# Kernel optimization log

Measured on AMD Instinct MI355X. Metric: run time of the kernel, lower is better.

Reference implementation:

```python
import jax, jax.numpy as jnp
import numpy as np

N = 131072   # nodes
C = 128      # in_channels
R = 4        # num_residues
H = 128      # hidden_channels
B = 1024     # graphs (segments)
QS = jnp.arange(1, 10, dtype=jnp.float32) * 0.1  # quantiles 0.1..0.9


def setup_inputs() -> dict:
    key = jax.random.key(0)
    ks = jax.random.split(key, 12)
    s = 0.05
    return {
        "embedding_0": jax.random.normal(ks[0], (N, C, 1, R), jnp.float32),
        "batch": jnp.sort(jax.random.randint(ks[1], (N,), 0, B, dtype=jnp.int32)),
        "W_lins": jax.random.normal(ks[2], (R - 1, C), jnp.float32) * s,
        "b_lins": jax.random.normal(ks[3], (R - 1,), jnp.float32) * s,
        "W1": jax.random.normal(ks[4], (C, H), jnp.float32) * s,
        "b1": jax.random.normal(ks[5], (H,), jnp.float32) * s,
        "W2": jax.random.normal(ks[6], (H,), jnp.float32) * s,
        "b2": jax.random.normal(ks[7], (1,), jnp.float32) * s,
        "Wm1": jax.random.normal(ks[8], (12, H), jnp.float32) * s,
        "bm1": jax.random.normal(ks[9], (H,), jnp.float32) * s,
        "Wm2": jax.random.normal(ks[10], (H,), jnp.float32) * s,
        "bm2": jax.random.normal(ks[11], (1,), jnp.float32) * s,
    }


def _node_readout(emb, W_lins, b_lins, W1, b1, W2, b2):
    x = emb[:, :, 0, :]                         # [N, C, R]
    # sum of (num_residues-1) plain linears, each Linear(C, 1)
    lin = jnp.einsum('ncr,rc->n', x[:, :, :-1], W_lins) + jnp.sum(b_lins)
    # non-linear branch on last residue: Linear(C,H) -> relu -> Linear(H,1)
    h = jax.nn.relu(x[:, :, -1] @ W1 + b1)      # [N, H]
    nl = h @ W2 + b2                            # [N]
    return lin + nl                             # [N]


def _multi_aggregate(v, batch):
    ones = jnp.ones_like(v)
    counts_f = jax.ops.segment_sum(ones, batch, num_segments=B)        # [B]
    counts = counts_f.astype(jnp.int32)
    safe_cnt = jnp.maximum(counts_f, 1.0)
    mean = jax.ops.segment_sum(v, batch, num_segments=B) / safe_cnt
    mx = jax.ops.segment_max(v, batch, num_segments=B)
    mn = jax.ops.segment_min(v, batch, num_segments=B)
    # per-segment sort (batch is primary key, value secondary)
    order = jnp.lexsort((v, batch))
    vs = v[order]                                                      # segment-sorted values
    offsets = jnp.concatenate([jnp.zeros(1, jnp.int32), jnp.cumsum(counts)[:-1].astype(jnp.int32)])
    last = offsets + jnp.maximum(counts, 1) - 1                        # last valid index per segment
    # linear-interpolated quantiles: pos = q*(count-1) within each segment
    pos = QS[:, None] * (safe_cnt[None, :] - 1.0)                      # [9, B]
    f = jnp.floor(pos).astype(jnp.int32)
    frac = pos - f.astype(jnp.float32)
    lo_idx = jnp.clip(offsets[None, :] + f, offsets[None, :], last[None, :])
    hi_idx = jnp.clip(lo_idx + 1, offsets[None, :], last[None, :])
    quant = vs[lo_idx] + frac * (vs[hi_idx] - vs[lo_idx])              # [9, B]
    nonempty = (counts > 0)[:, None]
    agg = jnp.concatenate([mean[:, None], mx[:, None], mn[:, None], quant.T], axis=1)  # [B, 12]
    return jnp.where(nonempty, agg, 0.0)


def reference(embedding_0, batch, W_lins, b_lins, W1, b1, W2, b2, Wm1, bm1, Wm2, bm2):
    batch = batch.astype(jnp.int32)
    v = _node_readout(embedding_0, W_lins, b_lins, W1, b1, W2, b2)     # [N]
    agg = _multi_aggregate(v, batch)                                   # [B, 12]
    out = jax.nn.relu(agg @ Wm1 + bm1) @ Wm2 + bm2                     # [B]
    return out
```

## Files before the change

kernel.cpp:

```cpp
#include <hip/hip_runtime.h>

#define N_NODES 131072
#define C_DIM   128
#define H_DIM   128
#define B_SEG   1024
#define M_TILE  128
#define K_TILE  32
#define YT_STR  132
#define SEGCAP  384

__global__ __launch_bounds__(256, 4)
void node_readout_kernel(const float* __restrict__ emb,
                         const float* __restrict__ W_lins,
                         const float* __restrict__ b_lins,
                         const float* __restrict__ W1,
                         const float* __restrict__ b1,
                         const float* __restrict__ W2,
                         const float* __restrict__ b2,
                         float* __restrict__ v_out)
{
    __shared__ float Yt[K_TILE * YT_STR];
    __shared__ float W1s[K_TILE * H_DIM];
    __shared__ float WLs[3 * C_DIM];
    __shared__ float lin_lds[M_TILE];

    const int t  = threadIdx.x;
    const int nbase = blockIdx.x * M_TILE;
    const int ln = t >> 5;
    const int cc = t & 31;
    const int jg = t & 15;
    const int mg = t >> 4;

    for (int i = t; i < 3 * C_DIM; i += 256) WLs[i] = W_lins[i];

    float acc[8][8];
    #pragma unroll
    for (int mi = 0; mi < 8; ++mi)
        #pragma unroll
        for (int ji = 0; ji < 8; ++ji) acc[mi][ji] = 0.0f;

    float lin_p[16];
    #pragma unroll
    for (int p = 0; p < 16; ++p) lin_p[p] = 0.0f;

    const float4* xbase = (const float4*)emb + (size_t)(nbase + ln) * C_DIM;
    const float4* W1_4  = (const float4*)W1;

    const int ct0 = (blockIdx.x ^ (blockIdx.x >> 8)) & 3;

    __syncthreads();

    for (int it = 0; it < C_DIM / K_TILE; ++it) {
        const int ct = (it + ct0) & 3;
        if (it) __syncthreads();

        float4 wr0 = W1_4[ct * 1024 + t];
        float4 wr1 = W1_4[ct * 1024 + t + 256];
        float4 wr2 = W1_4[ct * 1024 + t + 512];
        float4 wr3 = W1_4[ct * 1024 + t + 768];

        {
            const int c0 = ct * K_TILE + cc;
            const float wl0 = WLs[c0], wl1 = WLs[C_DIM + c0], wl2 = WLs[2 * C_DIM + c0];
            #pragma unroll
            for (int p = 0; p < 16; ++p) {
                float4 x = xbase[p * 8 * C_DIM + ct * K_TILE + cc];
                lin_p[p] = fmaf(x.x, wl0, fmaf(x.y, wl1, fmaf(x.z, wl2, lin_p[p])));
                Yt[cc * YT_STR + p * 8 + ln] = x.w;
            }
        }
        {
            float4* dst = (float4*)W1s;
            dst[t]       = wr0;
            dst[t + 256] = wr1;
            dst[t + 512] = wr2;
            dst[t + 768] = wr3;
        }
        __syncthreads();

        #pragma unroll 8
        for (int k = 0; k < K_TILE; ++k) {
            float4 ya = *(const float4*)&Yt[k * YT_STR + mg * 8];
            float4 yb = *(const float4*)&Yt[k * YT_STR + mg * 8 + 4];
            float w[8];
            #pragma unroll
            for (int ji = 0; ji < 8; ++ji) w[ji] = W1s[k * H_DIM + jg + 16 * ji];
            float ym[8] = {ya.x, ya.y, ya.z, ya.w, yb.x, yb.y, yb.z, yb.w};
            #pragma unroll
            for (int mi = 0; mi < 8; ++mi)
                #pragma unroll
                for (int ji = 0; ji < 8; ++ji)
                    acc[mi][ji] = fmaf(ym[mi], w[ji], acc[mi][ji]);
        }
    }

    #pragma unroll
    for (int p = 0; p < 16; ++p) {
        float s = lin_p[p];
        s += __shfl_xor(s, 16);
        s += __shfl_xor(s, 8);
        s += __shfl_xor(s, 4);
        s += __shfl_xor(s, 2);
        s += __shfl_xor(s, 1);
        lin_p[p] = s;
    }
    if (cc == 0) {
        #pragma unroll
        for (int p = 0; p < 16; ++p) lin_lds[p * 8 + ln] = lin_p[p];
    }

    __syncthreads();
    float* nl_red = W1s;

    float b1r[8], W2r[8];
    #pragma unroll
    for (int ji = 0; ji < 8; ++ji) {
        int j = jg + 16 * ji;
        b1r[ji] = b1[j];
        W2r[ji] = W2[j];
    }

    #pragma unroll
    for (int mi = 0; mi < 8; ++mi) {
        float s = 0.0f;
        #pragma unroll
        for (int ji = 0; ji < 8; ++ji) {
            float h = acc[mi][ji] + b1r[ji];
            h = h > 0.0f ? h : 0.0f;
            s = fmaf(h, W2r[ji], s);
        }
        nl_red[(mg * 8 + mi) * 17 + jg] = s;
    }
    __syncthreads();

    if (t < M_TILE) {
        float s = lin_lds[t];
        #pragma unroll
        for (int g = 0; g < 16; ++g) s += nl_red[t * 17 + g];
        s += b_lins[0] + b_lins[1] + b_lins[2] + b2[0];
        v_out[nbase + t] = s;
    }
}

__device__ __forceinline__ int lower_bound_wave(const int* __restrict__ batch,
                                                int target, int lane)
{
    int lo = 0, hi = N_NODES;
    while (lo < hi) {
        int span  = hi - lo;
        int chunk = (span + 63) >> 6;
        int idx   = lo + lane * chunk;
        bool p    = (idx < hi) && (batch[idx] < target);
        unsigned long long m = __ballot(p);
        int c = __popcll(m);
        if (c == 0) return lo;
        int nhi = (c < 64) ? (lo + c * chunk) : hi;
        lo = lo + (c - 1) * chunk + 1;
        hi = (nhi < hi) ? nhi : hi;
    }
    return lo;
}

__global__ __launch_bounds__(256)
void aggregate_kernel(const float* __restrict__ v,
                      const int* __restrict__ batch,
                      const float* __restrict__ Wm1,
                      const float* __restrict__ bm1,
                      const float* __restrict__ Wm2,
                      const float* __restrict__ bm2,
                      float* __restrict__ out)
{
    __shared__ float vals[4][SEGCAP];
    __shared__ float sorted[4][SEGCAP];
    __shared__ float agg_s[4][12];

    const int t    = threadIdx.x;
    const int wid  = t >> 6;
    const int lane = t & 63;
    const int b    = blockIdx.x * 4 + wid;

    const int start = lower_bound_wave(batch, b, lane);
    const int end   = lower_bound_wave(batch, b + 1, lane);
    int cnt = end - start;
    if (cnt > SEGCAP) cnt = SEGCAP;

    float lsum = 0.0f;
    for (int i = lane; i < cnt; i += 64) {
        float x = v[start + i];
        vals[wid][i] = x;
        lsum += x;
    }
    #pragma unroll
    for (int o = 32; o; o >>= 1) lsum += __shfl_xor(lsum, o);
    __syncthreads();

    for (int i = lane; i < cnt; i += 64) {
        float xi = vals[wid][i];
        int r = 0;
        for (int j = 0; j < cnt; ++j) {
            float xj = vals[wid][j];
            r += (xj < xi) || (xj == xi && j < i);
        }
        sorted[wid][r] = xi;
    }
    __syncthreads();

    if (cnt > 0) {
        float cntf = (float)cnt;
        if (lane == 9)  agg_s[wid][0] = lsum / cntf;
        if (lane == 10) agg_s[wid][1] = sorted[wid][cnt - 1];
        if (lane == 11) agg_s[wid][2] = sorted[wid][0];
        if (lane < 9) {
            float q   = (float)(lane + 1) * 0.1f;
            float pos = q * (cntf - 1.0f);
            float f   = floorf(pos);
            float frac = pos - f;
            int loi = (int)f;
            int hii = loi + 1; if (hii > cnt - 1) hii = cnt - 1;
            agg_s[wid][3 + lane] = sorted[wid][loi] + frac * (sorted[wid][hii] - sorted[wid][loi]);
        }
    } else {
        if (lane < 12) agg_s[wid][lane] = 0.0f;
    }
    __syncthreads();

    float term = 0.0f;
    #pragma unroll
    for (int rj = 0; rj < 2; ++rj) {
        int j = lane + 64 * rj;
        float h = bm1[j];
        #pragma unroll
        for (int k = 0; k < 12; ++k) h = fmaf(agg_s[wid][k], Wm1[k * H_DIM + j], h);
        h = h > 0.0f ? h : 0.0f;
        term = fmaf(h, Wm2[j], term);
    }
    #pragma unroll
    for (int o = 32; o; o >>= 1) term += __shfl_xor(term, o);
    if (lane == 0) out[b] = term + bm2[0];
}

extern "C" void kernel_launch(void* const* d_in, const int* in_sizes, int n_in,
                              void* d_out, int out_size, void* d_ws, size_t ws_size,
                              hipStream_t stream)
{
    const float* emb    = (const float*)d_in[0];
    const int*   batch  = (const int*)d_in[1];
    const float* W_lins = (const float*)d_in[2];
    const float* b_lins = (const float*)d_in[3];
    const float* W1     = (const float*)d_in[4];
    const float* b1     = (const float*)d_in[5];
    const float* W2     = (const float*)d_in[6];
    const float* b2     = (const float*)d_in[7];
    const float* Wm1    = (const float*)d_in[8];
    const float* bm1    = (const float*)d_in[9];
    const float* Wm2    = (const float*)d_in[10];
    const float* bm2    = (const float*)d_in[11];

    float* out  = (float*)d_out;
    float* vbuf = (float*)d_ws;

    node_readout_kernel<<<N_NODES / M_TILE, 256, 0, stream>>>(
        emb, W_lins, b_lins, W1, b1, W2, b2, vbuf);
    aggregate_kernel<<<B_SEG / 4, 256, 0, stream>>>(
        vbuf, batch, Wm1, bm1, Wm2, bm2, out);
}
```

Before: 423.0 us.

## Software-pipeline node readout with double-buffered Yt and register prefetch

```diff
diff --git a/kernel.cpp b/kernel.cpp
--- a/kernel.cpp
+++ b/kernel.cpp
@@ -9,7 +9,7 @@
 #define YT_STR  132
 #define SEGCAP  384
 
-__global__ __launch_bounds__(256, 4)
+__global__ __launch_bounds__(256, 3)
 void node_readout_kernel(const float* __restrict__ emb,
                          const float* __restrict__ W_lins,
                          const float* __restrict__ b_lins,
@@ -19,7 +19,7 @@
                          const float* __restrict__ b2,
                          float* __restrict__ v_out)
 {
-    __shared__ float Yt[K_TILE * YT_STR];
+    __shared__ float Yt[2][K_TILE * YT_STR];
     __shared__ float W1s[K_TILE * H_DIM];
     __shared__ float WLs[3 * C_DIM];
     __shared__ float lin_lds[M_TILE];
@@ -48,27 +48,41 @@
 
     const int ct0 = (blockIdx.x ^ (blockIdx.x >> 8)) & 3;
 
-    __syncthreads();
-
-    for (int it = 0; it < C_DIM / K_TILE; ++it) {
-        const int ct = (it + ct0) & 3;
-        if (it) __syncthreads();
-
-        float4 wr0 = W1_4[ct * 1024 + t];
-        float4 wr1 = W1_4[ct * 1024 + t + 256];
-        float4 wr2 = W1_4[ct * 1024 + t + 512];
-        float4 wr3 = W1_4[ct * 1024 + t + 768];
-
-        {
-            const int c0 = ct * K_TILE + cc;
-            const float wl0 = WLs[c0], wl1 = WLs[C_DIM + c0], wl2 = WLs[2 * C_DIM + c0];
-            #pragma unroll
-            for (int p = 0; p < 16; ++p) {
-                float4 x = xbase[p * 8 * C_DIM + ct * K_TILE + cc];
-                lin_p[p] = fmaf(x.x, wl0, fmaf(x.y, wl1, fmaf(x.z, wl2, lin_p[p])));
-                Yt[cc * YT_STR + p * 8 + ln] = x.w;
-            }
-        }
+    float4 wr0 = W1_4[ct0 * 1024 + t];
+    float4 wr1 = W1_4[ct0 * 1024 + t + 256];
+    float4 wr2 = W1_4[ct0 * 1024 + t + 512];
+    float4 wr3 = W1_4[ct0 * 1024 + t + 768];
+    float4 xp[8];
+    #pragma unroll
+    for (int p = 0; p < 8; ++p) xp[p] = xbase[p * 8 * C_DIM + ct0 * K_TILE + cc];
+
+    __syncthreads();
+
+    {
+        const int c0 = ct0 * K_TILE + cc;
+        const float wl0 = WLs[c0], wl1 = WLs[C_DIM + c0], wl2 = WLs[2 * C_DIM + c0];
+        #pragma unroll
+        for (int p = 0; p < 8; ++p) {
+            float4 x = xp[p];
+            lin_p[p] = fmaf(x.x, wl0, fmaf(x.y, wl1, fmaf(x.z, wl2, lin_p[p])));
+            Yt[0][cc * YT_STR + p * 8 + ln] = x.w;
+        }
+        #pragma unroll
+        for (int p = 0; p < 8; ++p) xp[p] = xbase[(p + 8) * 8 * C_DIM + ct0 * K_TILE + cc];
+        #pragma unroll
+        for (int p = 0; p < 8; ++p) {
+            float4 x = xp[p];
+            lin_p[p + 8] = fmaf(x.x, wl0, fmaf(x.y, wl1, fmaf(x.z, wl2, lin_p[p + 8])));
+            Yt[0][cc * YT_STR + (p + 8) * 8 + ln] = x.w;
+        }
+    }
+
+    for (int it = 0; it < 4; ++it) {
+        const int cur = it & 1;
+        const int ctn = (it + 1 + ct0) & 3;
+
+        __syncthreads();
+
         {
             float4* dst = (float4*)W1s;
             dst[t]       = wr0;
@@ -76,12 +90,20 @@
             dst[t + 512] = wr2;
             dst[t + 768] = wr3;
         }
+        if (it < 3) {
+            wr0 = W1_4[ctn * 1024 + t];
+            wr1 = W1_4[ctn * 1024 + t + 256];
+            wr2 = W1_4[ctn * 1024 + t + 512];
+            wr3 = W1_4[ctn * 1024 + t + 768];
+            #pragma unroll
+            for (int p = 0; p < 8; ++p) xp[p] = xbase[p * 8 * C_DIM + ctn * K_TILE + cc];
+        }
         __syncthreads();
 
         #pragma unroll 8
-        for (int k = 0; k < K_TILE; ++k) {
-            float4 ya = *(const float4*)&Yt[k * YT_STR + mg * 8];
-            float4 yb = *(const float4*)&Yt[k * YT_STR + mg * 8 + 4];
+        for (int k = 0; k < K_TILE / 2; ++k) {
+            float4 ya = *(const float4*)&Yt[cur][k * YT_STR + mg * 8];
+            float4 yb = *(const float4*)&Yt[cur][k * YT_STR + mg * 8 + 4];
             float w[8];
             #pragma unroll
             for (int ji = 0; ji < 8; ++ji) w[ji] = W1s[k * H_DIM + jg + 16 * ji];
@@ -91,6 +113,45 @@
                 #pragma unroll
                 for (int ji = 0; ji < 8; ++ji)
                     acc[mi][ji] = fmaf(ym[mi], w[ji], acc[mi][ji]);
+        }
+
+        if (it < 3) {
+            const int c0 = ctn * K_TILE + cc;
+            const float wl0 = WLs[c0], wl1 = WLs[C_DIM + c0], wl2 = WLs[2 * C_DIM + c0];
+            #pragma unroll
+            for (int p = 0; p < 8; ++p) {
+                float4 x = xp[p];
+                lin_p[p] = fmaf(x.x, wl0, fmaf(x.y, wl1, fmaf(x.z, wl2, lin_p[p])));
+                Yt[cur ^ 1][cc * YT_STR + p * 8 + ln] = x.w;
+            }
+            #pragma unroll
+            for (int p = 0; p < 8; ++p) xp[p] = xbase[(p + 8) * 8 * C_DIM + ctn * K_TILE + cc];
+        }
+
+        #pragma unroll 8
+        for (int k = K_TILE / 2; k < K_TILE; ++k) {
+            float4 ya = *(const float4*)&Yt[cur][k * YT_STR + mg * 8];
+            float4 yb = *(const float4*)&Yt[cur][k * YT_STR + mg * 8 + 4];
+            float w[8];
+            #pragma unroll
+            for (int ji = 0; ji < 8; ++ji) w[ji] = W1s[k * H_DIM + jg + 16 * ji];
+            float ym[8] = {ya.x, ya.y, ya.z, ya.w, yb.x, yb.y, yb.z, yb.w};
+            #pragma unroll
+            for (int mi = 0; mi < 8; ++mi)
+                #pragma unroll
+                for (int ji = 0; ji < 8; ++ji)
+                    acc[mi][ji] = fmaf(ym[mi], w[ji], acc[mi][ji]);
+        }
+
+        if (it < 3) {
+            const int c0 = ctn * K_TILE + cc;
+            const float wl0 = WLs[c0], wl1 = WLs[C_DIM + c0], wl2 = WLs[2 * C_DIM + c0];
+            #pragma unroll
+            for (int p = 0; p < 8; ++p) {
+                float4 x = xp[p];
+                lin_p[p + 8] = fmaf(x.x, wl0, fmaf(x.y, wl1, fmaf(x.z, wl2, lin_p[p + 8])));
+                Yt[cur ^ 1][cc * YT_STR + (p + 8) * 8 + ln] = x.w;
+            }
         }
     }
 
```

Measured after the change: 537.6 us. 1.27x slower.
